# Kernel optimization log

Measured on AMD Instinct MI355X. Metric: run time of the kernel, lower is better.

The kernel has to match this reference:

```python
import jax, jax.numpy as jnp
import numpy as np

N = 50000   # nodes
E = 300000  # directed edges (~Delaunay mesh, degree 6)
H = 128     # hidden_size
TW = 5      # time_window
P = 3       # process_steps
NODE_IN = 9
EDGE_IN = 4
LN_EPS = 1e-5


def _ln(x, g, b):
    m = jnp.mean(x, axis=-1, keepdims=True)
    v = jnp.var(x, axis=-1, keepdims=True)
    return (x - m) * jax.lax.rsqrt(v + LN_EPS) * g + b


def _mlp_ln(x, w1, b1, w2, b2, g, bb):
    # Linear -> ReLU -> Linear -> LayerNorm (matches MLP(..., layer_norm=True))
    h = jax.nn.relu(x @ w1 + b1)
    return _ln(h @ w2 + b2, g, bb)


def setup_inputs() -> dict:
    key = jax.random.key(0)
    ks = iter(jax.random.split(key, 64))
    def nrm(shape):
        return jax.random.normal(next(ks), shape, jnp.float32)
    def lin(fi, fo, stack=None):
        sh = (fi, fo) if stack is None else (stack, fi, fo)
        return nrm(sh) / np.sqrt(fi)
    inp = {}
    inp["temperature"] = nrm((N,))
    inp["temperature_prev"] = nrm((N,))
    inp["heat_source"] = nrm((N,))
    inp["heat_source_prev"] = nrm((N,))
    inp["heat_source_next"] = nrm((N, TW))
    inp["mesh_pos"] = jax.random.uniform(next(ks), (N, 2), jnp.float32)
    inp["edge_index"] = jax.random.randint(next(ks), (2, E), 0, N, jnp.int32)
    # Normalizer params (running mean/std)
    inp["node_norm_mean"] = jnp.zeros((NODE_IN,), jnp.float32)
    inp["node_norm_std"] = jnp.ones((NODE_IN,), jnp.float32)
    inp["edge_norm_mean"] = jnp.zeros((EDGE_IN,), jnp.float32)
    inp["edge_norm_std"] = jnp.ones((EDGE_IN,), jnp.float32)
    # node encoder
    inp["ne_w1"] = lin(NODE_IN, H); inp["ne_b1"] = jnp.zeros((H,), jnp.float32)
    inp["ne_w2"] = lin(H, H);       inp["ne_b2"] = jnp.zeros((H,), jnp.float32)
    inp["ne_g"] = jnp.ones((H,), jnp.float32); inp["ne_be"] = jnp.zeros((H,), jnp.float32)
    # edge encoder
    inp["ee_w1"] = lin(EDGE_IN, H); inp["ee_b1"] = jnp.zeros((H,), jnp.float32)
    inp["ee_w2"] = lin(H, H);       inp["ee_b2"] = jnp.zeros((H,), jnp.float32)
    inp["ee_g"] = jnp.ones((H,), jnp.float32); inp["ee_be"] = jnp.zeros((H,), jnp.float32)
    # processors (stacked over P steps): edge_mlp in=3H, node_mlp in=2H
    inp["pe_w1"] = lin(3 * H, H, P); inp["pe_b1"] = jnp.zeros((P, H), jnp.float32)
    inp["pe_w2"] = lin(H, H, P);     inp["pe_b2"] = jnp.zeros((P, H), jnp.float32)
    inp["pe_g"] = jnp.ones((P, H), jnp.float32); inp["pe_be"] = jnp.zeros((P, H), jnp.float32)
    inp["pn_w1"] = lin(2 * H, H, P); inp["pn_b1"] = jnp.zeros((P, H), jnp.float32)
    inp["pn_w2"] = lin(H, H, P);     inp["pn_b2"] = jnp.zeros((P, H), jnp.float32)
    inp["pn_g"] = jnp.ones((P, H), jnp.float32); inp["pn_be"] = jnp.zeros((P, H), jnp.float32)
    # decoder (Conv1d kernel_size=1 == per-node Linear), Swish in between
    inp["dec_w1"] = lin(H, H // 2); inp["dec_b1"] = jnp.zeros((H // 2,), jnp.float32)
    inp["dec_w2"] = lin(H // 2, TW); inp["dec_b2"] = jnp.zeros((TW,), jnp.float32)
    return inp


def reference(temperature, temperature_prev, heat_source, heat_source_prev,
              heat_source_next, mesh_pos, edge_index,
              node_norm_mean, node_norm_std, edge_norm_mean, edge_norm_std,
              ne_w1, ne_b1, ne_w2, ne_b2, ne_g, ne_be,
              ee_w1, ee_b1, ee_w2, ee_b2, ee_g, ee_be,
              pe_w1, pe_b1, pe_w2, pe_b2, pe_g, pe_be,
              pn_w1, pn_b1, pn_w2, pn_b2, pn_g, pn_be,
              dec_w1, dec_b1, dec_w2, dec_b2):
    u = temperature
    # node features: [u, u_dot, q, q_dot, q_next]  -> [N, 9]
    x = jnp.concatenate([
        u[:, None], (u - temperature_prev)[:, None],
        heat_source[:, None], (heat_source - heat_source_prev)[:, None],
        heat_source_next], axis=-1)
    s, r = edge_index[0], edge_index[1]  # senders (source j), receivers (target i)
    rel = mesh_pos[s] - mesh_pos[r]                       # [E, 2]
    dist = jnp.linalg.norm(rel, axis=-1, keepdims=True)   # [E, 1]
    relt = (u[s] - u[r])[:, None]                         # [E, 1]
    e = jnp.concatenate([rel, dist, relt], axis=-1)       # [E, 4]

    xh = _mlp_ln((x - node_norm_mean) / node_norm_std, ne_w1, ne_b1, ne_w2, ne_b2, ne_g, ne_be)
    eh = _mlp_ln((e - edge_norm_mean) / edge_norm_std, ee_w1, ee_b1, ee_w2, ee_b2, ee_g, ee_be)

    n_nodes = xh.shape[0]
    for i in range(P):
        xs, xr = xh[s], xh[r]  # x_j = x[source], x_i = x[target]
        # message: edge_mlp(cat[x_i, x_j, e]) then scatter-add at target index
        msg = _mlp_ln(jnp.concatenate([xr, xs, eh], axis=-1),
                      pe_w1[i], pe_b1[i], pe_w2[i], pe_b2[i], pe_g[i], pe_be[i])
        aggr = jax.ops.segment_sum(msg, r, num_segments=n_nodes)
        # node update + residual
        new_x = _mlp_ln(jnp.concatenate([aggr, xh], axis=-1),
                        pn_w1[i], pn_b1[i], pn_w2[i], pn_b2[i], pn_g[i], pn_be[i]) + xh
        # edge update (note row/col ordering differs from message) + residual
        new_e = _mlp_ln(jnp.concatenate([xs, xr, eh], axis=-1),
                        pe_w1[i], pe_b1[i], pe_w2[i], pe_b2[i], pe_g[i], pe_be[i]) + eh
        xh, eh = new_x, new_e

    # decoder: 1x1 convs == per-node linears, Swish(beta=1) activation
    h = xh @ dec_w1 + dec_b1
    h = h * jax.nn.sigmoid(h)
    delta = (h @ dec_w2 + dec_b2).reshape(-1, TW)
    dt = jnp.arange(1, TW + 1, dtype=delta.dtype)
    return dt[None, :] * delta
```

## Files before the change

kernel.cpp:

```cpp
#include <hip/hip_runtime.h>
#include <stdint.h>

typedef unsigned short u16;
typedef __attribute__((ext_vector_type(8))) short bf16x8_t;
typedef __attribute__((ext_vector_type(4))) float f32x4_t;

__device__ __forceinline__ float bl(u16 x) {
  union { unsigned u; float f; } c; c.u = ((unsigned)x) << 16; return c.f;
}
__device__ __forceinline__ u16 fb(float x) {
  union { float f; unsigned u; } c; c.f = x;
  unsigned r = c.u + 0x7fffu + ((c.u >> 16) & 1u);
  return (u16)(r >> 16);
}

__global__ void sentinel_kernel(float* out, int n) {
  int i = blockIdx.x * 256 + threadIdx.x;
  if (i < n) out[i] = 12345.f;
}

struct TSeg { const float* src; u16* dst; };
struct TArgs { TSeg s[23]; };
__global__ void transpose_w(TArgs a) {
  __shared__ u16 sT[128][132];
  const float* src = a.s[blockIdx.x].src;
  u16* dst = a.s[blockIdx.x].dst;
  for (int e = threadIdx.x; e < 16384; e += 256) {
    int k = e >> 7, n = e & 127;
    sT[n][k] = fb(src[e]);
  }
  __syncthreads();
  for (int e = threadIdx.x; e < 16384; e += 256) {
    int n = e >> 7, k = e & 127;
    dst[e] = sT[n][k];
  }
}

__global__ void transpose_w1d(const float* __restrict__ src, u16* __restrict__ dst) {
  __shared__ u16 sT[64][132];
  for (int e = threadIdx.x; e < 8192; e += 256) {
    int k = e >> 6, n = e & 63;
    sT[n][k] = fb(src[e]);
  }
  __syncthreads();
  for (int e = threadIdx.x; e < 8192; e += 256) {
    int n = e >> 7, k = e & 127;
    dst[e] = sT[n][k];
  }
}

__global__ void deg_count(const int* __restrict__ ei, int* __restrict__ cnt, int E) {
  int e = blockIdx.x * 256 + threadIdx.x;
  if (e < E) atomicAdd(&cnt[ei[E + e]], 1);
}
__global__ void scan1(const int* __restrict__ cnt, int* __restrict__ part,
                      int* __restrict__ bsum, int N) {
  __shared__ int s[256];
  int i = blockIdx.x * 256 + threadIdx.x;
  s[threadIdx.x] = (i < N) ? cnt[i] : 0;
  __syncthreads();
#pragma unroll
  for (int o = 1; o < 256; o <<= 1) {
    int t = (threadIdx.x >= o) ? s[threadIdx.x - o] : 0;
    __syncthreads();
    s[threadIdx.x] += t;
    __syncthreads();
  }
  if (i < N) part[i] = s[threadIdx.x];
  if (threadIdx.x == 255) bsum[blockIdx.x] = s[255];
}
__global__ void scan2(int* bsum, int nb) {
  __shared__ int s[256];
  __shared__ int carry;
  if (threadIdx.x == 0) carry = 0;
  __syncthreads();
  for (int base = 0; base < nb; base += 256) {
    int i = base + threadIdx.x;
    int v = (i < nb) ? bsum[i] : 0;
    s[threadIdx.x] = v;
    __syncthreads();
#pragma unroll
    for (int o = 1; o < 256; o <<= 1) {
      int t = (threadIdx.x >= o) ? s[threadIdx.x - o] : 0;
      __syncthreads();
      s[threadIdx.x] += t;
      __syncthreads();
    }
    int exc = s[threadIdx.x] - v + carry;
    if (i < nb) bsum[i] = exc;
    __syncthreads();
    if (threadIdx.x == 255) carry += s[255];
    __syncthreads();
  }
}
__global__ void scan3(const int* __restrict__ part, const int* __restrict__ bsum,
                      int* __restrict__ start, int N) {
  int i = blockIdx.x * 256 + threadIdx.x;
  if (i < N) start[i + 1] = part[i] + bsum[i >> 8];
  if (i == 0) start[0] = 0;
}
__global__ void fill_slot(const int* __restrict__ ei, int* __restrict__ cnt2,
                          const int* __restrict__ start, int* __restrict__ sortedS,
                          int* __restrict__ sortedR, int E) {
  int e = blockIdx.x * 256 + threadIdx.x;
  if (e >= E) return;
  int s = ei[e], r = ei[E + e];
  int p = atomicAdd(&cnt2[r], 1);
  int slot = start[r] + p;
  sortedS[slot] = s;
  sortedR[slot] = r;
}

template <int K, bool DUAL, bool NODE>
__global__ __launch_bounds__(256, 2) void encode_fused(
    const float* __restrict__ fa, const float* __restrict__ fb_, const float* __restrict__ fc,
    const float* __restrict__ fd, const float* __restrict__ fe,
    const float* __restrict__ fmean, const float* __restrict__ fstd,
    const int* __restrict__ sArr, const int* __restrict__ rArr,
    const float* __restrict__ w1f, const float* __restrict__ b1f,
    const u16* __restrict__ wt2, const float* __restrict__ b2, const float* __restrict__ gg,
    const float* __restrict__ bb, u16* __restrict__ out,
    const u16* __restrict__ wtA2, const u16* __restrict__ wtB2, u16* __restrict__ xhA,
    u16* __restrict__ xhB, float* __restrict__ aggr, int M) {
  __shared__ float sW1[K * 128];
  __shared__ float sB1[128];
  __shared__ float sM[16], sS[16];
  __shared__ u16 sH[64][136];
  __shared__ u16 sO1[DUAL ? 64 : 1][136];
  const int tid = threadIdx.x;
  const int wave = tid >> 6, lane = tid & 63;
  const int q = lane >> 4, l16 = lane & 15;
  const int m0 = blockIdx.x * 64;
  const int rowb = wave * 16 + q * 4;
  const int arow = m0 + wave * 16 + l16;
  const int arc = arow < M ? arow : M - 1;

  float rv[4], rq[5];
  int s_, r_;
  if constexpr (NODE) {
    rv[0] = fa[arc]; rv[1] = fb_[arc]; rv[2] = fc[arc]; rv[3] = fd[arc];
#pragma unroll
    for (int j = 0; j < 5; ++j) rq[j] = fe[(size_t)arc * 5 + j];
  } else {
    s_ = sArr[arc]; r_ = rArr[arc];
    rv[0] = fa[s_ * 2] - fa[r_ * 2];
    rv[1] = fa[s_ * 2 + 1] - fa[r_ * 2 + 1];
    rv[2] = fb_[s_];
    rv[3] = fb_[r_];
  }

  for (int i = tid; i < K * 128; i += 256) sW1[i] = w1f[i];
  if (tid < 128) sB1[tid] = b1f[tid];
  if (tid < K) { sM[tid] = fmean[tid]; sS[tid] = fstd[tid]; }
  __syncthreads();

  float fr[K];
  if constexpr (NODE) {
    float x[9];
    x[0] = rv[0]; x[1] = rv[0] - rv[1];
    x[2] = rv[2]; x[3] = rv[2] - rv[3];
#pragma unroll
    for (int j = 0; j < 5; ++j) x[4 + j] = rq[j];
#pragma unroll
    for (int k = 0; k < 9; ++k) fr[k] = (x[k] - sM[k]) / sS[k];
  } else {
    float d = sqrtf(rv[0] * rv[0] + rv[1] * rv[1]);
    float x[4] = {rv[0], rv[1], d, rv[2] - rv[3]};
#pragma unroll
    for (int k = 0; k < 4; ++k) fr[k] = (x[k] - sM[k]) / sS[k];
  }

  f32x4_t acc[8];
#pragma unroll
  for (int b = 0; b < 8; ++b) acc[b] = (f32x4_t){0.f, 0.f, 0.f, 0.f};
#pragma unroll
  for (int kk = 0; kk < 4; ++kk) {
    union { u16 u[8]; bf16x8_t v; } cv;
#pragma unroll
    for (int j = 0; j < 8; ++j) {
      int col = kk * 32 + q * 8 + j;
      float h = sB1[col];
#pragma unroll
      for (int k = 0; k < K; ++k) h += fr[k] * sW1[k * 128 + col];
      cv.u[j] = fb(h > 0.f ? h : 0.f);
    }
#pragma unroll
    for (int nt = 0; nt < 8; ++nt) {
      bf16x8_t bfv = *(const bf16x8_t*)(wt2 + (size_t)(nt * 16 + l16) * 128 + kk * 32 + q * 8);
      acc[nt] = __builtin_amdgcn_mfma_f32_16x16x32_bf16(cv.v, bfv, acc[nt], 0, 0, 0);
    }
  }

  float bcol[8], gcol[8], becol[8];
#pragma unroll
  for (int nt = 0; nt < 8; ++nt) {
    bcol[nt] = b2[nt * 16 + l16];
    gcol[nt] = gg[nt * 16 + l16];
    becol[nt] = bb[nt * 16 + l16];
  }
  float s[4] = {0, 0, 0, 0}, ss[4] = {0, 0, 0, 0};
#pragma unroll
  for (int r = 0; r < 4; ++r)
#pragma unroll
    for (int nt = 0; nt < 8; ++nt) {
      float v = acc[nt][r] + bcol[nt];
      s[r] += v;
      ss[r] += v * v;
    }
#pragma unroll
  for (int r = 0; r < 4; ++r) {
#pragma unroll
    for (int m = 1; m <= 8; m <<= 1) {
      s[r] += __shfl_xor(s[r], m, 64);
      ss[r] += __shfl_xor(ss[r], m, 64);
    }
  }
#pragma unroll
  for (int r = 0; r < 4; ++r) {
    float mean = s[r] * (1.f / 128.f);
    float var = fmaxf(ss[r] * (1.f / 128.f) - mean * mean, 0.f);
    float rstd = rsqrtf(var + 1e-5f);
#pragma unroll
    for (int nt = 0; nt < 8; ++nt) {
      float v = (acc[nt][r] + bcol[nt] - mean) * rstd * gcol[nt] + becol[nt];
      sH[rowb + r][nt * 16 + l16] = fb(v);
    }
  }
  __syncthreads();
#pragma unroll
  for (int it = 0; it < 4; ++it) {
    int lin = it * 256 + tid;
    int row = lin >> 4, ch = (lin & 15) * 8;
    int grow = m0 + row;
    if (grow >= M) continue;
    *(uint4*)(out + (size_t)grow * 128 + ch) = *(uint4*)(&sH[row][ch]);
  }

  if constexpr (DUAL) {
    {
      float4 z = make_float4(0.f, 0.f, 0.f, 0.f);
#pragma unroll
      for (int it = 0; it < 8; ++it) {
        int lin = it * 256 + tid;
        int row = lin >> 5, c4 = (lin & 31) * 4;
        int grow = m0 + row;
        if (grow < M) *(float4*)(aggr + (size_t)grow * 128 + c4) = z;
      }
    }
    f32x4_t a0[8], a1[8];
#pragma unroll
    for (int b = 0; b < 8; ++b) {
      a0[b] = (f32x4_t){0.f, 0.f, 0.f, 0.f};
      a1[b] = (f32x4_t){0.f, 0.f, 0.f, 0.f};
    }
#pragma unroll
    for (int kk = 0; kk < 4; ++kk) {
      bf16x8_t af = *(const bf16x8_t*)(&sH[wave * 16 + l16][kk * 32 + q * 8]);
#pragma unroll
      for (int nt = 0; nt < 8; ++nt) {
        bf16x8_t b0 = *(const bf16x8_t*)(wtA2 + (size_t)(nt * 16 + l16) * 128 + kk * 32 + q * 8);
        bf16x8_t b1v = *(const bf16x8_t*)(wtB2 + (size_t)(nt * 16 + l16) * 128 + kk * 32 + q * 8);
        a0[nt] = __builtin_amdgcn_mfma_f32_16x16x32_bf16(af, b0, a0[nt], 0, 0, 0);
        a1[nt] = __builtin_amdgcn_mfma_f32_16x16x32_bf16(af, b1v, a1[nt], 0, 0, 0);
      }
    }
    __syncthreads();
#pragma unroll
    for (int r = 0; r < 4; ++r)
#pragma unroll
      for (int nt = 0; nt < 8; ++nt) {
        sH[rowb + r][nt * 16 + l16] = fb(a0[nt][r]);
        sO1[rowb + r][nt * 16 + l16] = fb(a1[nt][r]);
      }
    __syncthreads();
#pragma unroll
    for (int it = 0; it < 4; ++it) {
      int lin = it * 256 + tid;
      int row = lin >> 4, ch = (lin & 15) * 8;
      int grow = m0 + row;
      if (grow >= M) continue;
      *(uint4*)(xhA + (size_t)grow * 128 + ch) = *(uint4*)(&sH[row][ch]);
      *(uint4*)(xhB + (size_t)grow * 128 + ch) = *(uint4*)(&sO1[row][ch]);
    }
  }
}

template <bool DEC>
__global__ __launch_bounds__(256, 2) void node_fused_2w(
    u16* __restrict__ xh, float* __restrict__ aggr, const u16* __restrict__ wtA,
    const u16* __restrict__ wtB, const float* __restrict__ b1, const u16* __restrict__ wt2,
    const float* __restrict__ b2, const float* __restrict__ gg, const float* __restrict__ bb,
    const u16* __restrict__ wtA2, const u16* __restrict__ wtB2, u16* __restrict__ xhA,
    u16* __restrict__ xhB,
    const u16* __restrict__ w1t, const float* __restrict__ db1,
    const float* __restrict__ w2d, const float* __restrict__ db2, float* __restrict__ outp,
    int M) {
  __shared__ u16 sH[64][136];
  __shared__ u16 sO1[DEC ? 1 : 64][136];
  __shared__ float sW2d[DEC ? 320 : 1];
  __shared__ float sDb1[DEC ? 64 : 1];
  const int tid = threadIdx.x;
  const int wave = tid >> 6, lane = tid & 63;
  const int q = lane >> 4, l16 = lane & 15;
  const int m0 = blockIdx.x * 64;
  const int rowb = wave * 16 + q * 4;
  const int arow = m0 + wave * 16 + l16;
  const int arc = arow < M ? arow : M - 1;

  if constexpr (DEC) {
    for (int i = tid; i < 320; i += 256) sW2d[i] = w2d[i];
    if (tid < 64) sDb1[tid] = db1[tid];
  }

  bf16x8_t xf[4], af_[4];
#pragma unroll
  for (int kk = 0; kk < 4; ++kk) {
    xf[kk] = *(const bf16x8_t*)(xh + (size_t)arc * 128 + kk * 32 + q * 8);
    const float* ap = aggr + (size_t)arc * 128 + kk * 32 + q * 8;
    union { u16 u[8]; bf16x8_t v; } cv;
#pragma unroll
    for (int j = 0; j < 8; ++j) cv.u[j] = fb(ap[j]);
    af_[kk] = cv.v;
  }

  f32x4_t acc[8];
#pragma unroll
  for (int b = 0; b < 8; ++b) acc[b] = (f32x4_t){0.f, 0.f, 0.f, 0.f};
#pragma unroll
  for (int kk = 0; kk < 4; ++kk) {
#pragma unroll
    for (int nt = 0; nt < 8; ++nt) {
      bf16x8_t bA = *(const bf16x8_t*)(wtA + (size_t)(nt * 16 + l16) * 128 + kk * 32 + q * 8);
      bf16x8_t bB = *(const bf16x8_t*)(wtB + (size_t)(nt * 16 + l16) * 128 + kk * 32 + q * 8);
      acc[nt] = __builtin_amdgcn_mfma_f32_16x16x32_bf16(af_[kk], bA, acc[nt], 0, 0, 0);
      acc[nt] = __builtin_amdgcn_mfma_f32_16x16x32_bf16(xf[kk], bB, acc[nt], 0, 0, 0);
    }
  }
  float bcol1[8];
#pragma unroll
  for (int nt = 0; nt < 8; ++nt) bcol1[nt] = b1[nt * 16 + l16];
#pragma unroll
  for (int r = 0; r < 4; ++r)
#pragma unroll
    for (int nt = 0; nt < 8; ++nt) {
      float v = acc[nt][r] + bcol1[nt];
      sH[rowb + r][nt * 16 + l16] = fb(v > 0.f ? v : 0.f);
    }
  __syncthreads();

  f32x4_t acc2[8];
#pragma unroll
  for (int b = 0; b < 8; ++b) acc2[b] = (f32x4_t){0.f, 0.f, 0.f, 0.f};
#pragma unroll
  for (int kk = 0; kk < 4; ++kk) {
    bf16x8_t afm = *(const bf16x8_t*)(&sH[wave * 16 + l16][kk * 32 + q * 8]);
#pragma unroll
    for (int nt = 0; nt < 8; ++nt) {
      bf16x8_t bfv = *(const bf16x8_t*)(wt2 + (size_t)(nt * 16 + l16) * 128 + kk * 32 + q * 8);
      acc2[nt] = __builtin_amdgcn_mfma_f32_16x16x32_bf16(afm, bfv, acc2[nt], 0, 0, 0);
    }
  }
  float bcol[8], gcol[8], becol[8];
#pragma unroll
  for (int nt = 0; nt < 8; ++nt) {
    bcol[nt] = b2[nt * 16 + l16];
    gcol[nt] = gg[nt * 16 + l16];
    becol[nt] = bb[nt * 16 + l16];
  }
  float s[4] = {0, 0, 0, 0}, ss[4] = {0, 0, 0, 0};
#pragma unroll
  for (int r = 0; r < 4; ++r)
#pragma unroll
    for (int nt = 0; nt < 8; ++nt) {
      float v = acc2[nt][r] + bcol[nt];
      s[r] += v;
      ss[r] += v * v;
    }
#pragma unroll
  for (int r = 0; r < 4; ++r) {
#pragma unroll
    for (int m = 1; m <= 8; m <<= 1) {
      s[r] += __shfl_xor(s[r], m, 64);
      ss[r] += __shfl_xor(ss[r], m, 64);
    }
  }
  __syncthreads();
#pragma unroll
  for (int r = 0; r < 4; ++r) {
    float mean = s[r] * (1.f / 128.f);
    float var = fmaxf(ss[r] * (1.f / 128.f) - mean * mean, 0.f);
    float rstd = rsqrtf(var + 1e-5f);
#pragma unroll
    for (int nt = 0; nt < 8; ++nt) {
      float v = (acc2[nt][r] + bcol[nt] - mean) * rstd * gcol[nt] + becol[nt];
      sH[rowb + r][nt * 16 + l16] = fb(v);
    }
  }
  __syncthreads();

  bf16x8_t nf[4];
#pragma unroll
  for (int kk = 0; kk < 4; ++kk) {
    u16 y8[8];
    *(uint4*)y8 = *(uint4*)(&sH[wave * 16 + l16][kk * 32 + q * 8]);
#pragma unroll
    for (int j = 0; j < 8; ++j) y8[j] = fb(bl(y8[j]) + bl((u16)xf[kk][j]));
    nf[kk] = *(bf16x8_t*)y8;
    if constexpr (!DEC) {
      if (arow < M)
        *(uint4*)(xh + (size_t)arow * 128 + kk * 32 + q * 8) = *(uint4*)y8;
    }
  }

  if constexpr (DEC) {
    __syncthreads();
    float* sHf = (float*)&sH[0][0];
    f32x4_t dacc[4];
#pragma unroll
    for (int b = 0; b < 4; ++b) dacc[b] = (f32x4_t){0.f, 0.f, 0.f, 0.f};
#pragma unroll
    for (int kk = 0; kk < 4; ++kk) {
#pragma unroll
      for (int nt = 0; nt < 4; ++nt) {
        bf16x8_t bfv = *(const bf16x8_t*)(w1t + (size_t)(nt * 16 + l16) * 128 + kk * 32 + q * 8);
        dacc[nt] = __builtin_amdgcn_mfma_f32_16x16x32_bf16(nf[kk], bfv, dacc[nt], 0, 0, 0);
      }
    }
#pragma unroll
    for (int r = 0; r < 4; ++r)
#pragma unroll
      for (int nt = 0; nt < 4; ++nt) {
        float h = dacc[nt][r] + sDb1[nt * 16 + l16];
        float hs = h * (1.f / (1.f + __expf(-h)));
        sHf[(rowb + r) * 68 + nt * 16 + l16] = hs;
      }
    __syncthreads();
    int row = tid >> 2, tq = tid & 3;
    int grow = m0 + row;
    if (grow < M) {
#pragma unroll
      for (int t0 = 0; t0 < 2; ++t0) {
        int t = (t0 == 0) ? tq : (tq == 0 ? 4 : -1);
        if (t < 0) continue;
        float p = db2[t];
        for (int k = 0; k < 64; ++k) p += sHf[row * 68 + k] * sW2d[k * 5 + t];
        outp[(size_t)grow * 5 + t] = (float)(t + 1) * p;
      }
    }
    return;
  }

  if (wtA2 == nullptr) return;

  if (arow < M) {
    float4 z = make_float4(0.f, 0.f, 0.f, 0.f);
#pragma unroll
    for (int kk = 0; kk < 4; ++kk) {
      *(float4*)(aggr + (size_t)arow * 128 + kk * 32 + q * 8) = z;
      *(float4*)(aggr + (size_t)arow * 128 + kk * 32 + q * 8 + 4) = z;
    }
  }

  f32x4_t a0[8], a1[8];
#pragma unroll
  for (int b = 0; b < 8; ++b) {
    a0[b] = (f32x4_t){0.f, 0.f, 0.f, 0.f};
    a1[b] = (f32x4_t){0.f, 0.f, 0.f, 0.f};
  }
#pragma unroll
  for (int kk = 0; kk < 4; ++kk) {
#pragma unroll
    for (int nt = 0; nt < 8; ++nt) {
      bf16x8_t b0 = *(const bf16x8_t*)(wtA2 + (size_t)(nt * 16 + l16) * 128 + kk * 32 + q * 8);
      bf16x8_t b1v = *(const bf16x8_t*)(wtB2 + (size_t)(nt * 16 + l16) * 128 + kk * 32 + q * 8);
      a0[nt] = __builtin_amdgcn_mfma_f32_16x16x32_bf16(nf[kk], b0, a0[nt], 0, 0, 0);
      a1[nt] = __builtin_amdgcn_mfma_f32_16x16x32_bf16(nf[kk], b1v, a1[nt], 0, 0, 0);
    }
  }
  __syncthreads();
#pragma unroll
  for (int r = 0; r < 4; ++r)
#pragma unroll
    for (int nt = 0; nt < 8; ++nt) {
      sH[rowb + r][nt * 16 + l16] = fb(a0[nt][r]);
      sO1[rowb + r][nt * 16 + l16] = fb(a1[nt][r]);
    }
  __syncthreads();
#pragma unroll
  for (int it = 0; it < 4; ++it) {
    int lin = it * 256 + tid;
    int row = lin >> 4, ch = (lin & 15) * 8;
    int grow = m0 + row;
    if (grow >= M) continue;
    *(uint4*)(xhA + (size_t)grow * 128 + ch) = *(uint4*)(&sH[row][ch]);
    *(uint4*)(xhB + (size_t)grow * 128 + ch) = *(uint4*)(&sO1[row][ch]);
  }
}

template <bool CSR, bool LAST>
__global__ __launch_bounds__(256, 2) void edge_fused(
    u16* __restrict__ eh, const u16* __restrict__ xhA, const u16* __restrict__ xhB,
    const u16* __restrict__ wtC, const float* __restrict__ b1, const u16* __restrict__ wt2,
    const float* __restrict__ b2, const float* __restrict__ gg, const float* __restrict__ bb,
    const int* __restrict__ sArr, const int* __restrict__ rArr,
    const int* __restrict__ startp, float* __restrict__ aggr, int E) {
  __shared__ u16 sHm[64][136];
  __shared__ u16 sHe[LAST ? 1 : 64][136];
  __shared__ int sR[64];
  __shared__ float sB1[128];
  const int tid = threadIdx.x;
  const int wave = tid >> 6, lane = tid & 63;
  const int q = lane >> 4, l16 = lane & 15;
  const int m0 = blockIdx.x * 64;
  const int rowb = wave * 16 + q * 4;
  int arow = m0 + wave * 16 + l16;
  int arc = arow < E ? arow : E - 1;

  if (tid < 64) {
    int e = m0 + tid;
    sR[tid] = (e < E) ? rArr[e] : -1;
  }
  if (tid < 128) sB1[tid] = b1[tid];

  int psv[4], prv[4];
#pragma unroll
  for (int it = 0; it < 4; ++it) {
    int lin = it * 256 + tid;
    int ge = m0 + (lin >> 4);
    int gc = ge < E ? ge : E - 1;
    psv[it] = sArr[gc];
    prv[it] = rArr[gc];
  }

  bf16x8_t ehf[4];
#pragma unroll
  for (int kk = 0; kk < 4; ++kk)
    ehf[kk] = *(const bf16x8_t*)(eh + (size_t)arc * 128 + kk * 32 + q * 8);

  f32x4_t accC[8];
#pragma unroll
  for (int b = 0; b < 8; ++b) accC[b] = (f32x4_t){0.f, 0.f, 0.f, 0.f};
#pragma unroll
  for (int kk = 0; kk < 4; ++kk) {
#pragma unroll
    for (int nt = 0; nt < 8; ++nt) {
      bf16x8_t bfv = *(const bf16x8_t*)(wtC + (size_t)(nt * 16 + l16) * 128 + kk * 32 + q * 8);
      accC[nt] = __builtin_amdgcn_mfma_f32_16x16x32_bf16(ehf[kk], bfv, accC[nt], 0, 0, 0);
    }
  }
  __builtin_amdgcn_sched_barrier(0);

  uint4 pAr[4], pBs[4], pAs[4], pBr[4];
#pragma unroll
  for (int it = 0; it < 4; ++it) {
    int ch = ((it * 256 + tid) & 15) * 8;
    pAr[it] = *(const uint4*)(xhA + (size_t)prv[it] * 128 + ch);
    pBs[it] = *(const uint4*)(xhB + (size_t)psv[it] * 128 + ch);
    if constexpr (!LAST) {
      pAs[it] = *(const uint4*)(xhA + (size_t)psv[it] * 128 + ch);
      pBr[it] = *(const uint4*)(xhB + (size_t)prv[it] * 128 + ch);
    }
  }

#pragma unroll
  for (int r = 0; r < 4; ++r)
#pragma unroll
    for (int nt = 0; nt < 8; ++nt) sHm[rowb + r][nt * 16 + l16] = fb(accC[nt][r]);
  __syncthreads();

#pragma unroll
  for (int it = 0; it < 4; ++it) {
    int lin = it * 256 + tid;
    int row = lin >> 4, ch = (lin & 15) * 8;
    bool ok = (m0 + row) < E;
    u16 t8[8], ar[8], as_[8], br[8], bs[8], hm[8], he[8];
    *(uint4*)t8 = *(uint4*)(&sHm[row][ch]);
    *(uint4*)ar = pAr[it];
    *(uint4*)bs = pBs[it];
    if constexpr (!LAST) {
      *(uint4*)as_ = pAs[it];
      *(uint4*)br = pBr[it];
    }
#pragma unroll
    for (int j = 0; j < 8; ++j) {
      float t = bl(t8[j]) + sB1[ch + j];
      float vm = t + bl(ar[j]) + bl(bs[j]);
      hm[j] = (ok && vm > 0.f) ? fb(vm) : 0;
      if constexpr (!LAST) {
        float ve = t + bl(as_[j]) + bl(br[j]);
        he[j] = (ok && ve > 0.f) ? fb(ve) : 0;
      }
    }
    *(uint4*)(&sHm[row][ch]) = *(uint4*)hm;
    if constexpr (!LAST) *(uint4*)(&sHe[row][ch]) = *(uint4*)he;
  }
  __syncthreads();

  float bcol[8], gcol[8], becol[8];
#pragma unroll
  for (int nt = 0; nt < 8; ++nt) {
    bcol[nt] = b2[nt * 16 + l16];
    gcol[nt] = gg[nt * 16 + l16];
    becol[nt] = bb[nt * 16 + l16];
  }

  f32x4_t accM[8], accE[8];
#pragma unroll
  for (int b = 0; b < 8; ++b) {
    accM[b] = (f32x4_t){0.f, 0.f, 0.f, 0.f};
    accE[b] = (f32x4_t){0.f, 0.f, 0.f, 0.f};
  }
#pragma unroll
  for (int kk = 0; kk < 4; ++kk) {
    bf16x8_t afm = *(const bf16x8_t*)(&sHm[wave * 16 + l16][kk * 32 + q * 8]);
    bf16x8_t afe;
    if constexpr (!LAST) afe = *(const bf16x8_t*)(&sHe[wave * 16 + l16][kk * 32 + q * 8]);
#pragma unroll
    for (int nt = 0; nt < 8; ++nt) {
      bf16x8_t bfv = *(const bf16x8_t*)(wt2 + (size_t)(nt * 16 + l16) * 128 + kk * 32 + q * 8);
      accM[nt] = __builtin_amdgcn_mfma_f32_16x16x32_bf16(afm, bfv, accM[nt], 0, 0, 0);
      if constexpr (!LAST)
        accE[nt] = __builtin_amdgcn_mfma_f32_16x16x32_bf16(afe, bfv, accE[nt], 0, 0, 0);
    }
  }
  float sm[4] = {0, 0, 0, 0}, ssm[4] = {0, 0, 0, 0};
  float se[4] = {0, 0, 0, 0}, sse[4] = {0, 0, 0, 0};
#pragma unroll
  for (int r = 0; r < 4; ++r)
#pragma unroll
    for (int nt = 0; nt < 8; ++nt) {
      float vm = accM[nt][r] + bcol[nt];
      sm[r] += vm; ssm[r] += vm * vm;
      if constexpr (!LAST) {
        float ve = accE[nt][r] + bcol[nt];
        se[r] += ve; sse[r] += ve * ve;
      }
    }
#pragma unroll
  for (int r = 0; r < 4; ++r) {
#pragma unroll
    for (int m = 1; m <= 8; m <<= 1) {
      sm[r] += __shfl_xor(sm[r], m, 64);
      ssm[r] += __shfl_xor(ssm[r], m, 64);
      if constexpr (!LAST) {
        se[r] += __shfl_xor(se[r], m, 64);
        sse[r] += __shfl_xor(sse[r], m, 64);
      }
    }
  }

  if (!CSR) {
#pragma unroll
    for (int r = 0; r < 4; ++r) {
      int row = m0 + rowb + r;
      if (row >= E) continue;
      int rr = sR[rowb + r];
      float mean = sm[r] * (1.f / 128.f);
      float var = fmaxf(ssm[r] * (1.f / 128.f) - mean * mean, 0.f);
      float rstd = rsqrtf(var + 1e-5f);
#pragma unroll
      for (int nt = 0; nt < 8; ++nt) {
        float v = (accM[nt][r] + bcol[nt] - mean) * rstd * gcol[nt] + becol[nt];
        atomicAdd(&aggr[(size_t)rr * 128 + nt * 16 + l16], v);
      }
    }
  }

  __syncthreads();
#pragma unroll
  for (int r = 0; r < 4; ++r) {
    float meanM = sm[r] * (1.f / 128.f);
    float varM = fmaxf(ssm[r] * (1.f / 128.f) - meanM * meanM, 0.f);
    float rstdM = rsqrtf(varM + 1e-5f);
    if constexpr (!LAST) {
      float meanE = se[r] * (1.f / 128.f);
      float varE = fmaxf(sse[r] * (1.f / 128.f) - meanE * meanE, 0.f);
      float rstdE = rsqrtf(varE + 1e-5f);
#pragma unroll
      for (int nt = 0; nt < 8; ++nt) {
        float ve = (accE[nt][r] + bcol[nt] - meanE) * rstdE * gcol[nt] + becol[nt];
        sHe[rowb + r][nt * 16 + l16] = fb(ve);
      }
    }
    if (CSR) {
#pragma unroll
      for (int nt = 0; nt < 8; ++nt) {
        float vm = (accM[nt][r] + bcol[nt] - meanM) * rstdM * gcol[nt] + becol[nt];
        sHm[rowb + r][nt * 16 + l16] = fb(vm);
      }
    }
  }
  __syncthreads();

#pragma unroll
  for (int it = 0; it < 4; ++it) {
    int lin = it * 256 + tid;
    int row = lin >> 4, ch = (lin & 15) * 8;
    int grow = m0 + row;
    if (grow >= E) continue;
    if constexpr (!LAST) {
      u16 y8[8], e8[8];
      *(uint4*)y8 = *(uint4*)(&sHe[row][ch]);
      *(uint4*)e8 = *(const uint4*)(eh + (size_t)grow * 128 + ch);
#pragma unroll
      for (int j = 0; j < 8; ++j) y8[j] = fb(bl(y8[j]) + bl(e8[j]));
      *(uint4*)(eh + (size_t)grow * 128 + ch) = *(uint4*)y8;
    }

    if (CSR) {
      int rr = sR[row];
      if (rr < 0) continue;
      bool first = (row == 0) || (sR[row - 1] != rr);
      if (!first) continue;
      int gs = startp[rr], ge2 = startp[rr + 1];
      int le = ge2 - m0;
      if (le > 64) le = 64;
      float acc[8] = {0, 0, 0, 0, 0, 0, 0, 0};
      for (int i = row; i < le; ++i) {
        u16 m8[8];
        *(uint4*)m8 = *(uint4*)(&sHm[i][ch]);
#pragma unroll
        for (int j = 0; j < 8; ++j) acc[j] += bl(m8[j]);
      }
      if (gs >= m0 && ge2 <= m0 + 64) {
        *(float4*)(aggr + (size_t)rr * 128 + ch) = make_float4(acc[0], acc[1], acc[2], acc[3]);
        *(float4*)(aggr + (size_t)rr * 128 + ch + 4) =
            make_float4(acc[4], acc[5], acc[6], acc[7]);
      } else {
#pragma unroll
        for (int j = 0; j < 8; ++j) atomicAdd(&aggr[(size_t)rr * 128 + ch + j], acc[j]);
      }
    }
  }
}

extern "C" void kernel_launch(void* const* d_in, const int* in_sizes, int n_in, void* d_out,
                              int out_size, void* d_ws, size_t ws_size, hipStream_t stream) {
  auto F = [&](int i) { return (const float*)d_in[i]; };
  const int* edge_index = (const int*)d_in[6];
  const int N_ = in_sizes[0];
  const int E_ = in_sizes[6] / 2;

  char* wsb = (char*)d_ws;
  size_t off = 0;
  auto alloc = [&](size_t bytes) -> char* {
    char* p = wsb + off;
    off += (bytes + 255) & ~(size_t)255;
    return p;
  };
  u16* xh = (u16*)alloc((size_t)N_ * 128 * 2);
  u16* xhA = (u16*)alloc((size_t)N_ * 128 * 2);
  u16* xhB = (u16*)alloc((size_t)N_ * 128 * 2);
  u16* ehP = (u16*)alloc((size_t)E_ * 128 * 2);
  float* aggr = (float*)alloc((size_t)N_ * 128 * 4);
  u16* wne2T = (u16*)alloc(16384 * 2);
  u16* wee2T = (u16*)alloc(16384 * 2);
  u16* wpe1T = (u16*)alloc((size_t)9 * 16384 * 2);
  u16* wpe2T = (u16*)alloc((size_t)3 * 16384 * 2);
  u16* wpn1T = (u16*)alloc((size_t)6 * 16384 * 2);
  u16* wpn2T = (u16*)alloc((size_t)3 * 16384 * 2);
  u16* w1dT = (u16*)alloc(8192 * 2);

  const size_t base_off = off;
  int* startp = (int*)alloc((size_t)(N_ + 1) * 4);
  int* cntp = (int*)alloc((size_t)N_ * 4);
  int* partp = (int*)alloc((size_t)N_ * 4);
  int* bsump = (int*)alloc(((size_t)(N_ + 255) / 256) * 4 + 256);
  int* sortedS = (int*)alloc((size_t)E_ * 4);
  int* sortedR = (int*)alloc((size_t)E_ * 4);
  bool useCSR = (off <= ws_size);
  if (!useCSR) {
    off = base_off;
    if (off > ws_size) {
      sentinel_kernel<<<(out_size + 255) / 256, 256, 0, stream>>>((float*)d_out, out_size);
      return;
    }
  }

  TArgs ta;
  int ts = 0;
  ta.s[ts++] = {F(13), wne2T};
  ta.s[ts++] = {F(19), wee2T};
  for (int i = 0; i < 3; ++i)
    for (int b = 0; b < 3; ++b)
      ta.s[ts++] = {F(23) + (size_t)(i * 3 + b) * 16384, wpe1T + (size_t)(i * 3 + b) * 16384};
  for (int i = 0; i < 3; ++i) ta.s[ts++] = {F(25) + (size_t)i * 16384, wpe2T + (size_t)i * 16384};
  for (int i = 0; i < 3; ++i)
    for (int b = 0; b < 2; ++b)
      ta.s[ts++] = {F(29) + (size_t)(i * 2 + b) * 16384, wpn1T + (size_t)(i * 2 + b) * 16384};
  for (int i = 0; i < 3; ++i) ta.s[ts++] = {F(31) + (size_t)i * 16384, wpn2T + (size_t)i * 16384};

  const int tilesN = (N_ + 63) / 64;
  const int tilesE = (E_ + 63) / 64;
  const int nb = (N_ + 255) / 256;
  dim3 blk(256);

  transpose_w<<<23, blk, 0, stream>>>(ta);
  transpose_w1d<<<1, blk, 0, stream>>>(F(35), w1dT);

  const int* sArr = edge_index;
  const int* rArr = edge_index + E_;
  if (useCSR) {
    hipMemsetAsync(cntp, 0, (size_t)N_ * 4, stream);
    deg_count<<<(E_ + 255) / 256, blk, 0, stream>>>(edge_index, cntp, E_);
    scan1<<<nb, blk, 0, stream>>>(cntp, partp, bsump, N_);
    scan2<<<1, blk, 0, stream>>>(bsump, nb);
    scan3<<<nb, blk, 0, stream>>>(partp, bsump, startp, N_);
    hipMemsetAsync(cntp, 0, (size_t)N_ * 4, stream);
    fill_slot<<<(E_ + 255) / 256, blk, 0, stream>>>(edge_index, cntp, startp, sortedS, sortedR,
                                                    E_);
    sArr = sortedS;
    rArr = sortedR;
  }

  encode_fused<4, false, false><<<tilesE, blk, 0, stream>>>(
      F(5), F(0), nullptr, nullptr, nullptr, F(9), F(10), sArr, rArr,
      F(17), F(18), wee2T, F(20), F(21), F(22), ehP,
      nullptr, nullptr, nullptr, nullptr, nullptr, E_);
  encode_fused<9, true, true><<<tilesN, blk, 0, stream>>>(
      F(0), F(1), F(2), F(3), F(4), F(7), F(8), nullptr, nullptr,
      F(11), F(12), wne2T, F(14), F(15), F(16), xh,
      wpe1T, wpe1T + 16384, xhA, xhB, aggr, N_);

  for (int i = 0; i < 3; ++i) {
    const u16* wtC = wpe1T + (size_t)(i * 3 + 2) * 16384;
    const float* pb1 = F(24) + i * 128;
    const u16* wt2 = wpe2T + (size_t)i * 16384;
    const float* pb2 = F(26) + i * 128;
    const float* pg = F(27) + i * 128;
    const float* pbe = F(28) + i * 128;
    const u16* wtnA = wpn1T + (size_t)(i * 2 + 0) * 16384;
    const u16* wtnB = wpn1T + (size_t)(i * 2 + 1) * 16384;
    const float* nb1 = F(30) + i * 128;
    const u16* wtn2 = wpn2T + (size_t)i * 16384;
    const float* nb2 = F(32) + i * 128;
    const float* ng = F(33) + i * 128;
    const float* nbe = F(34) + i * 128;

    const bool last = (i == 2);
    if (useCSR) {
      if (last)
        edge_fused<true, true><<<tilesE, blk, 0, stream>>>(ehP, xhA, xhB, wtC, pb1, wt2, pb2,
                                                           pg, pbe, sArr, rArr, startp, aggr, E_);
      else
        edge_fused<true, false><<<tilesE, blk, 0, stream>>>(ehP, xhA, xhB, wtC, pb1, wt2, pb2,
                                                            pg, pbe, sArr, rArr, startp, aggr, E_);
    } else {
      if (last)
        edge_fused<false, true><<<tilesE, blk, 0, stream>>>(ehP, xhA, xhB, wtC, pb1, wt2, pb2,
                                                            pg, pbe, sArr, rArr, nullptr, aggr, E_);
      else
        edge_fused<false, false><<<tilesE, blk, 0, stream>>>(ehP, xhA, xhB, wtC, pb1, wt2, pb2,
                                                             pg, pbe, sArr, rArr, nullptr, aggr, E_);
    }
    if (last) {
      node_fused_2w<true><<<tilesN, blk, 0, stream>>>(
          xh, aggr, wtnA, wtnB, nb1, wtn2, nb2, ng, nbe,
          nullptr, nullptr, nullptr, nullptr,
          w1dT, F(36), F(37), F(38), (float*)d_out, N_);
    } else {
      const u16* wtA2 = wpe1T + (size_t)((i + 1) * 3 + 0) * 16384;
      const u16* wtB2 = wpe1T + (size_t)((i + 1) * 3 + 1) * 16384;
      node_fused_2w<false><<<tilesN, blk, 0, stream>>>(
          xh, aggr, wtnA, wtnB, nb1, wtn2, nb2, ng, nbe,
          wtA2, wtB2, xhA, xhB,
          nullptr, nullptr, nullptr, nullptr, nullptr, N_);
    }
  }
}
```

Baseline: 1.104 ms.

## Fuse edge encoder into first processor edge kernel

Drops the separate edge encoder launch and computes the edge features, encoder MLP and LayerNorm inside the first edge_fused step. The encoded edge state is written to global memory for later steps, while the first step reads its MFMA operands straight from shared memory instead of re-reading eh. This removes one kernel launch and one global read pass over the edge hidden state. The cost is more shared memory and registers in the ENC variant, which may lower occupancy.

```diff
diff --git a/kernel.cpp b/kernel.cpp
--- a/kernel.cpp
+++ b/kernel.cpp
@@ -497,17 +497,25 @@
   }
 }
 
-template <bool CSR, bool LAST>
+template <bool CSR, bool LAST, bool ENC>
 __global__ __launch_bounds__(256, 2) void edge_fused(
     u16* __restrict__ eh, const u16* __restrict__ xhA, const u16* __restrict__ xhB,
     const u16* __restrict__ wtC, const float* __restrict__ b1, const u16* __restrict__ wt2,
     const float* __restrict__ b2, const float* __restrict__ gg, const float* __restrict__ bb,
     const int* __restrict__ sArr, const int* __restrict__ rArr,
-    const int* __restrict__ startp, float* __restrict__ aggr, int E) {
+    const int* __restrict__ startp, float* __restrict__ aggr,
+    const float* __restrict__ ew1, const float* __restrict__ eb1,
+    const u16* __restrict__ ewt2, const float* __restrict__ eb2,
+    const float* __restrict__ eg, const float* __restrict__ ebe,
+    const float* __restrict__ emean, const float* __restrict__ estd,
+    const float* __restrict__ mp, const float* __restrict__ tarr, int E) {
   __shared__ u16 sHm[64][136];
   __shared__ u16 sHe[LAST ? 1 : 64][136];
   __shared__ int sR[64];
   __shared__ float sB1[128];
+  __shared__ float sW1e[ENC ? 512 : 1];
+  __shared__ float sB1e[ENC ? 128 : 1];
+  __shared__ float sMS[ENC ? 8 : 1];
   const int tid = threadIdx.x;
   const int wave = tid >> 6, lane = tid & 63;
   const int q = lane >> 4, l16 = lane & 15;
@@ -533,9 +541,92 @@
   }
 
   bf16x8_t ehf[4];
-#pragma unroll
-  for (int kk = 0; kk < 4; ++kk)
-    ehf[kk] = *(const bf16x8_t*)(eh + (size_t)arc * 128 + kk * 32 + q * 8);
+  if constexpr (ENC) {
+    for (int i = tid; i < 512; i += 256) sW1e[i] = ew1[i];
+    if (tid < 128) sB1e[tid] = eb1[tid];
+    if (tid < 4) { sMS[tid] = emean[tid]; sMS[4 + tid] = estd[tid]; }
+    int es = sArr[arc], er = rArr[arc];
+    float r0 = mp[es * 2] - mp[er * 2];
+    float r1 = mp[es * 2 + 1] - mp[er * 2 + 1];
+    float r2 = tarr[es], r3 = tarr[er];
+    __syncthreads();
+    float dd = sqrtf(r0 * r0 + r1 * r1);
+    float fx[4] = {r0, r1, dd, r2 - r3};
+    float fr[4];
+#pragma unroll
+    for (int k = 0; k < 4; ++k) fr[k] = (fx[k] - sMS[k]) / sMS[4 + k];
+
+    f32x4_t eacc[8];
+#pragma unroll
+    for (int b = 0; b < 8; ++b) eacc[b] = (f32x4_t){0.f, 0.f, 0.f, 0.f};
+#pragma unroll
+    for (int kk = 0; kk < 4; ++kk) {
+      union { u16 u[8]; bf16x8_t v; } cv;
+#pragma unroll
+      for (int j = 0; j < 8; ++j) {
+        int col = kk * 32 + q * 8 + j;
+        float h = sB1e[col];
+#pragma unroll
+        for (int k = 0; k < 4; ++k) h += fr[k] * sW1e[k * 128 + col];
+        cv.u[j] = fb(h > 0.f ? h : 0.f);
+      }
+#pragma unroll
+      for (int nt = 0; nt < 8; ++nt) {
+        bf16x8_t bfv =
+            *(const bf16x8_t*)(ewt2 + (size_t)(nt * 16 + l16) * 128 + kk * 32 + q * 8);
+        eacc[nt] = __builtin_amdgcn_mfma_f32_16x16x32_bf16(cv.v, bfv, eacc[nt], 0, 0, 0);
+      }
+    }
+    float s0[4] = {0, 0, 0, 0}, ss0[4] = {0, 0, 0, 0};
+    float eb2c[8];
+#pragma unroll
+    for (int nt = 0; nt < 8; ++nt) eb2c[nt] = eb2[nt * 16 + l16];
+#pragma unroll
+    for (int r = 0; r < 4; ++r)
+#pragma unroll
+      for (int nt = 0; nt < 8; ++nt) {
+        float v = eacc[nt][r] + eb2c[nt];
+        s0[r] += v;
+        ss0[r] += v * v;
+      }
+#pragma unroll
+    for (int r = 0; r < 4; ++r) {
+#pragma unroll
+      for (int m = 1; m <= 8; m <<= 1) {
+        s0[r] += __shfl_xor(s0[r], m, 64);
+        ss0[r] += __shfl_xor(ss0[r], m, 64);
+      }
+    }
+#pragma unroll
+    for (int r = 0; r < 4; ++r) {
+      float mean = s0[r] * (1.f / 128.f);
+      float var = fmaxf(ss0[r] * (1.f / 128.f) - mean * mean, 0.f);
+      float rstd = rsqrtf(var + 1e-5f);
+#pragma unroll
+      for (int nt = 0; nt < 8; ++nt) {
+        int col = nt * 16 + l16;
+        float v = (eacc[nt][r] + eb2c[nt] - mean) * rstd * eg[col] + ebe[col];
+        sHm[rowb + r][col] = fb(v);
+      }
+    }
+    __syncthreads();
+#pragma unroll
+    for (int it = 0; it < 4; ++it) {
+      int lin = it * 256 + tid;
+      int row = lin >> 4, ch = (lin & 15) * 8;
+      int grow = m0 + row;
+      if (grow >= E) continue;
+      *(uint4*)(eh + (size_t)grow * 128 + ch) = *(uint4*)(&sHm[row][ch]);
+    }
+#pragma unroll
+    for (int kk = 0; kk < 4; ++kk)
+      ehf[kk] = *(const bf16x8_t*)(&sHm[wave * 16 + l16][kk * 32 + q * 8]);
+    __syncthreads();
+  } else {
+#pragma unroll
+    for (int kk = 0; kk < 4; ++kk)
+      ehf[kk] = *(const bf16x8_t*)(eh + (size_t)arc * 128 + kk * 32 + q * 8);
+  }
 
   f32x4_t accC[8];
 #pragma unroll
@@ -813,10 +904,6 @@
     rArr = sortedR;
   }
 
-  encode_fused<4, false, false><<<tilesE, blk, 0, stream>>>(
-      F(5), F(0), nullptr, nullptr, nullptr, F(9), F(10), sArr, rArr,
-      F(17), F(18), wee2T, F(20), F(21), F(22), ehP,
-      nullptr, nullptr, nullptr, nullptr, nullptr, E_);
   encode_fused<9, true, true><<<tilesN, blk, 0, stream>>>(
       F(0), F(1), F(2), F(3), F(4), F(7), F(8), nullptr, nullptr,
       F(11), F(12), wne2T, F(14), F(15), F(16), xh,
@@ -837,23 +924,39 @@
     const float* ng = F(33) + i * 128;
     const float* nbe = F(34) + i * 128;
 
-    const bool last = (i == 2);
     if (useCSR) {
-      if (last)
-        edge_fused<true, true><<<tilesE, blk, 0, stream>>>(ehP, xhA, xhB, wtC, pb1, wt2, pb2,
-                                                           pg, pbe, sArr, rArr, startp, aggr, E_);
+      if (i == 0)
+        edge_fused<true, false, true><<<tilesE, blk, 0, stream>>>(
+            ehP, xhA, xhB, wtC, pb1, wt2, pb2, pg, pbe, sArr, rArr, startp, aggr,
+            F(17), F(18), wee2T, F(20), F(21), F(22), F(9), F(10), F(5), F(0), E_);
+      else if (i == 1)
+        edge_fused<true, false, false><<<tilesE, blk, 0, stream>>>(
+            ehP, xhA, xhB, wtC, pb1, wt2, pb2, pg, pbe, sArr, rArr, startp, aggr,
+            nullptr, nullptr, nullptr, nullptr, nullptr, nullptr, nullptr, nullptr,
+            nullptr, nullptr, E_);
       else
-        edge_fused<true, false><<<tilesE, blk, 0, stream>>>(ehP, xhA, xhB, wtC, pb1, wt2, pb2,
-                                                            pg, pbe, sArr, rArr, startp, aggr, E_);
+        edge_fused<true, true, false><<<tilesE, blk, 0, stream>>>(
+            ehP, xhA, xhB, wtC, pb1, wt2, pb2, pg, pbe, sArr, rArr, startp, aggr,
+            nullptr, nullptr, nullptr, nullptr, nullptr, nullptr, nullptr, nullptr,
+            nullptr, nullptr, E_);
     } else {
-      if (last)
-        edge_fused<false, true><<<tilesE, blk, 0, stream>>>(ehP, xhA, xhB, wtC, pb1, wt2, pb2,
-                                                            pg, pbe, sArr, rArr, nullptr, aggr, E_);
+      if (i == 0)
+        edge_fused<false, false, true><<<tilesE, blk, 0, stream>>>(
+            ehP, xhA, xhB, wtC, pb1, wt2, pb2, pg, pbe, sArr, rArr, nullptr, aggr,
+            F(17), F(18), wee2T, F(20), F(21), F(22), F(9), F(10), F(5), F(0), E_);
+      else if (i == 1)
+        edge_fused<false, false, false><<<tilesE, blk, 0, stream>>>(
+            ehP, xhA, xhB, wtC, pb1, wt2, pb2, pg, pbe, sArr, rArr, nullptr, aggr,
+            nullptr, nullptr, nullptr, nullptr, nullptr, nullptr, nullptr, nullptr,
+            nullptr, nullptr, E_);
       else
-        edge_fused<false, false><<<tilesE, blk, 0, stream>>>(ehP, xhA, xhB, wtC, pb1, wt2, pb2,
-                                                             pg, pbe, sArr, rArr, nullptr, aggr, E_);
-    }
-    if (last) {
+        edge_fused<false, true, false><<<tilesE, blk, 0, stream>>>(
+            ehP, xhA, xhB, wtC, pb1, wt2, pb2, pg, pbe, sArr, rArr, nullptr, aggr,
+            nullptr, nullptr, nullptr, nullptr, nullptr, nullptr, nullptr, nullptr,
+            nullptr, nullptr, E_);
+    }
+
+    if (i == 2) {
       node_fused_2w<true><<<tilesN, blk, 0, stream>>>(
           xh, aggr, wtnA, wtnB, nb1, wtn2, nb2, ng, nbe,
           nullptr, nullptr, nullptr, nullptr,
```

Result: slower. 1.130 ms (+2.4%).
